# Performance work log

Hardware: AMD Instinct MI355X
Metric: run time of the kernel (lower is better)

Reference implementation:

```python
import jax, jax.numpy as jnp
import numpy as np

B, S, V, D = 64, 256, 50000, 300
NW, CL, CV, CD = 8192, 16, 500, 30
H, T, CH = 128, 17, 30


def setup_inputs() -> dict:
    key = jax.random.key(0)
    ks = jax.random.split(key, 32)
    f32 = jnp.float32
    def rn(k, shape, scale=0.1):
        return jax.random.normal(k, shape, dtype=f32) * scale
    inp = {}
    inp["char_emb"] = rn(ks[0], (CV, CD)).at[0].set(0.0)  # padding_idx=0
    inp["conv_w"] = rn(ks[1], (CH, CD, 3))  # OIH
    inp["conv_b"] = rn(ks[2], (CH,))
    inp["word_emb"] = rn(ks[3], (V, D))
    in0, in1 = D + CH, 2 * H
    inp["w_ih_l0"] = rn(ks[4], (2, 3 * H, in0))  # [dir, 3H, in]
    inp["w_hh_l0"] = rn(ks[5], (2, 3 * H, H))
    inp["b_ih_l0"] = rn(ks[6], (2, 3 * H))
    inp["b_hh_l0"] = rn(ks[7], (2, 3 * H))
    inp["w_ih_l1"] = rn(ks[8], (2, 3 * H, in1))
    inp["w_hh_l1"] = rn(ks[9], (2, 3 * H, H))
    inp["b_ih_l1"] = rn(ks[10], (2, 3 * H))
    inp["b_hh_l1"] = rn(ks[11], (2, 3 * H))
    inp["mlp_w1"] = rn(ks[12], (2 * H, H))
    inp["mlp_b1"] = rn(ks[13], (H,))
    inp["mlp_w2"] = rn(ks[14], (H, T))
    inp["mlp_b2"] = rn(ks[15], (T,))
    inp["crf_start"] = rn(ks[16], (T,))
    inp["crf_end"] = rn(ks[17], (T,))
    inp["crf_trans"] = rn(ks[18], (T, T))
    inp["batched_char_words"] = jax.random.randint(ks[19], (NW, CL), 0, CV)
    inp["batched_char_words_len"] = jax.random.randint(ks[20], (NW,), 1, CL + 1)
    inp["batched_char_word_index"] = jax.random.randint(ks[21], (B, S), 0, NW + 1)
    inp["batched_tokens"] = jax.random.randint(ks[22], (B, S), 0, V)
    inp["batched_tokens_len"] = jax.random.randint(ks[23], (B,), S // 2, S + 1)
    inp["target"] = jax.random.randint(ks[24], (B, S), 0, T)
    return inp


def _gru_dir(x, mask, w_ih, w_hh, b_ih, b_hh, reverse):
    # x: [B,S,I], mask: [B,S] bool. Masked (padded) steps carry hidden state
    # through unchanged, matching pack_padded_sequence semantics.
    xg = jnp.einsum('bsi,gi->sbg', x, w_ih) + b_ih  # [S,B,3H]
    m = mask.T  # [S,B]
    h0 = jnp.zeros((x.shape[0], w_hh.shape[1]), x.dtype)

    def step(h, inp):
        xt, mt = inp
        hg = h @ w_hh.T + b_hh
        xr, xz, xn = jnp.split(xt, 3, axis=-1)
        hr, hz, hn = jnp.split(hg, 3, axis=-1)
        r = jax.nn.sigmoid(xr + hr)
        z = jax.nn.sigmoid(xz + hz)
        n = jnp.tanh(xn + r * hn)
        hnew = (1.0 - z) * n + z * h
        h = jnp.where(mt[:, None], hnew, h)
        return h, h

    _, hs = jax.lax.scan(step, h0, (xg, m), reverse=reverse)
    return hs.transpose(1, 0, 2)  # [B,S,H]


def _bigru_layer(x, mask, w_ih, w_hh, b_ih, b_hh):
    fwd = _gru_dir(x, mask, w_ih[0], w_hh[0], b_ih[0], b_hh[0], False)
    bwd = _gru_dir(x, mask, w_ih[1], w_hh[1], b_ih[1], b_hh[1], True)
    return jnp.concatenate([fwd, bwd], axis=-1)


def _forward(char_emb, conv_w, conv_b, word_emb,
             w_ih_l0, w_hh_l0, b_ih_l0, b_hh_l0,
             w_ih_l1, w_hh_l1, b_ih_l1, b_hh_l1,
             mlp_w1, mlp_b1, mlp_w2, mlp_b2,
             crf_start, crf_end, crf_trans,
             batched_char_words, batched_char_word_index,
             batched_tokens, batched_tokens_len, target):
    # --- char CNN token encoder: conv1d(k=3, SAME) + relu + max-over-time ---
    ct = char_emb[batched_char_words]  # [NW,CL,CD]
    c = jax.lax.conv_general_dilated(ct.transpose(0, 2, 1), conv_w, (1,), 'SAME',
                                     dimension_numbers=('NCH', 'OIH', 'NCH'))
    c = jax.nn.relu(c + conv_b[None, :, None])
    tok_enc = jnp.max(c, axis=-1)  # [NW,CH]
    tok_enc = jnp.concatenate([jnp.zeros((1, tok_enc.shape[1]), tok_enc.dtype), tok_enc], axis=0)
    tok_idx = tok_enc[batched_char_word_index]  # [B,S,CH] (index 0 -> zeros)

    texts = jnp.concatenate([word_emb[batched_tokens], tok_idx], axis=-1)  # [B,S,D+CH]
    seq = batched_tokens.shape[1]
    mask = jnp.arange(seq)[None, :] < batched_tokens_len[:, None]  # [B,S]

    # --- 2-layer BiGRU ---
    h = _bigru_layer(texts, mask, w_ih_l0, w_hh_l0, b_ih_l0, b_hh_l0)
    h = _bigru_layer(h, mask, w_ih_l1, w_hh_l1, b_ih_l1, b_hh_l1)

    # --- MLP head -> emissions [B,S,17] ---
    h = jax.nn.relu(h @ mlp_w1 + mlp_b1)
    emissions = h @ mlp_w2 + mlp_b2

    # --- CRF negative log-likelihood, reduction='token_mean' ---
    maskf = mask.astype(emissions.dtype)
    emit_sc = jnp.take_along_axis(emissions, target[..., None], axis=-1)[..., 0]  # [B,S]
    trans_sc = crf_trans[target[:, :-1], target[:, 1:]]  # [B,S-1]
    score = crf_start[target[:, 0]] + emit_sc[:, 0]
    score = score + jnp.sum((trans_sc + emit_sc[:, 1:]) * maskf[:, 1:], axis=1)
    last_tags = jnp.take_along_axis(target, (batched_tokens_len - 1)[:, None], axis=1)[:, 0]
    score = score + crf_end[last_tags]

    alpha0 = crf_start[None, :] + emissions[:, 0]  # [B,T]
    em_rest = emissions[:, 1:].transpose(1, 0, 2)  # [S-1,B,T]
    m_rest = mask[:, 1:].T  # [S-1,B]

    def crf_step(alpha, inp):
        emit, mt = inp
        new = jax.nn.logsumexp(alpha[:, :, None] + crf_trans[None], axis=1) + emit
        return jnp.where(mt[:, None], new, alpha), None

    alpha, _ = jax.lax.scan(crf_step, alpha0, (em_rest, m_rest))
    log_z = jax.nn.logsumexp(alpha + crf_end[None, :], axis=1)
    llh = score - log_z
    return -(jnp.sum(llh) / jnp.sum(maskf))


def reference(char_emb, conv_w, conv_b, word_emb,
              w_ih_l0, w_hh_l0, b_ih_l0, b_hh_l0,
              w_ih_l1, w_hh_l1, b_ih_l1, b_hh_l1,
              mlp_w1, mlp_b1, mlp_w2, mlp_b2,
              crf_start, crf_end, crf_trans,
              batched_char_words, batched_char_words_len,
              batched_char_word_index, batched_tokens, batched_tokens_len, target):
    return _forward(char_emb, conv_w, conv_b, word_emb,
                    w_ih_l0, w_hh_l0, b_ih_l0, b_hh_l0,
                    w_ih_l1, w_hh_l1, b_ih_l1, b_hh_l1,
                    mlp_w1, mlp_b1, mlp_w2, mlp_b2,
                    crf_start, crf_end, crf_trans,
                    batched_char_words, batched_char_word_index,
                    batched_tokens, batched_tokens_len, target)
```

## Files before the change

### kernel.cpp

```cpp
#include <hip/hip_runtime.h>
#include <cstddef>

#define BATCH 64
#define SEQ   256
#define VOCAB 50000
#define DIM   300
#define NW    8192
#define CLEN  16
#define CDIM  30
#define CHC   30
#define HID   128
#define NT    17
#define IN0   (DIM + CHC)
#define IN0P  336
#define IN1   (2 * HID)
#define NPOS  (BATCH * SEQ)

constexpr size_t SZ_XG    = 2ull * BATCH * SEQ * 384;
constexpr size_t SZ_TEXTS = (size_t)NPOS * IN0P;
constexpr size_t SZ_H1    = (size_t)NPOS * 256;
constexpr size_t SZ_TOK   = 245792;
constexpr size_t SZ_EMIS  = (size_t)NPOS * NT;
constexpr size_t SZ_WPAD  = 768ull * IN0P;
constexpr size_t OFF_XG    = 0;
constexpr size_t OFF_TEXTS = OFF_XG + SZ_XG;
constexpr size_t OFF_H1    = OFF_TEXTS + SZ_TEXTS;
constexpr size_t OFF_TOK   = OFF_H1 + SZ_H1;
constexpr size_t OFF_EMIS  = OFF_TOK + SZ_TOK;
constexpr size_t OFF_WPAD  = OFF_EMIS + SZ_EMIS;
constexpr size_t OFF_LLH   = OFF_WPAD + SZ_WPAD;

__device__ __forceinline__ float sigm(float x) {
    return 1.f / (1.f + __expf(-x));
}
__device__ __forceinline__ float tanh_fast(float x) {
    x = fminf(fmaxf(x, -15.f), 15.f);
    float e = __expf(-2.f * x);
    return (1.f - e) / (1.f + e);
}
__device__ __forceinline__ float quad_sum(float x) {
    int y = __builtin_amdgcn_update_dpp(0, __float_as_int(x), 0xB1, 0xF, 0xF, false);
    x += __int_as_float(y);
    y = __builtin_amdgcn_update_dpp(0, __float_as_int(x), 0x4E, 0xF, 0xF, false);
    x += __int_as_float(y);
    return x;
}

__global__ __launch_bounds__(256) void char_conv_k(
    const float* __restrict__ char_emb,
    const float* __restrict__ conv_w,
    const float* __restrict__ conv_b,
    const int*   __restrict__ words,
    float* __restrict__ tok_enc)
{
    __shared__ __align__(16) float cs[8][CLEN][CDIM];
    __shared__ float wsm[CHC * CDIM * 3];
    __shared__ float bs[CHC];
    int n0 = blockIdx.x * 8;
    int tid = threadIdx.x;
    for (int e = tid; e < CHC * CDIM * 3; e += 256) wsm[e] = conv_w[e];
    if (tid < CHC) bs[tid] = conv_b[tid];
    for (int e = tid; e < 8 * CLEN * CDIM; e += 256) {
        int wi = e / (CLEN * CDIM);
        int rem = e - wi * (CLEN * CDIM);
        int l = rem / CDIM;
        int i = rem - l * CDIM;
        int ci = words[(n0 + wi) * CLEN + l];
        cs[wi][l][i] = char_emb[ci * CDIM + i];
    }
    __syncthreads();
    int wi = tid >> 5;
    int o = tid & 31;
    if (o < CHC) {
        float best = -1e30f;
        for (int l = 0; l < CLEN; l++) {
            float s = 0.f;
            #pragma unroll
            for (int k = 0; k < 3; k++) {
                int ll = l + k - 1;
                if (ll >= 0 && ll < CLEN) {
                    #pragma unroll
                    for (int i = 0; i < CDIM; i++)
                        s += cs[wi][ll][i] * wsm[(o * CDIM + i) * 3 + k];
                }
            }
            best = fmaxf(best, s);
        }
        tok_enc[(size_t)(n0 + wi + 1) * CDIM + o] = fmaxf(best + bs[o], 0.f);
    }
}

__global__ __launch_bounds__(128) void build_texts_k(
    const float* __restrict__ word_emb,
    const float* __restrict__ tok_enc,
    const int*   __restrict__ tokens,
    const int*   __restrict__ widx,
    float* __restrict__ texts)
{
    int p = blockIdx.x;
    int tok = tokens[p];
    int ci = widx[p];
    float* o = texts + (size_t)p * IN0P;
    const float* wr = word_emb + (size_t)tok * DIM;
    const float* tr = tok_enc + (size_t)ci * CDIM;
    for (int c = threadIdx.x; c < IN0P; c += 128)
        o[c] = (c < DIM) ? wr[c] : (c < IN0 ? tr[c - DIM] : 0.f);
}

__global__ __launch_bounds__(64) void pad_w_k(
    const float* __restrict__ w, float* __restrict__ wp)
{
    int r = blockIdx.x;
    for (int c = threadIdx.x; c < IN0P; c += 64)
        wp[(size_t)r * IN0P + c] = (c < IN0) ? w[(size_t)r * IN0 + c] : 0.f;
}

#define GBM 128
#define GBN 128
#define GBK 16
__global__ __launch_bounds__(256, 3) void gemm_xg_k(
    const float* __restrict__ A,
    const float* __restrict__ W,
    const float* __restrict__ bias,
    float* __restrict__ out,
    int K)
{
    __shared__ __align__(16) float As[2][GBK][GBM];
    __shared__ __align__(16) float Ws[2][GBK][GBN];
    int tid = threadIdx.x;
    int n0 = blockIdx.x * GBN;
    int m0 = blockIdx.y * GBM;
    int lrow = tid >> 1;
    int lk = (tid & 1) * 8;
    int ty = tid >> 4;
    int tx = tid & 15;

    const float* ap = A + (size_t)(m0 + lrow) * K + lk;
    const float* wpt = W + (size_t)(n0 + lrow) * K + lk;

    float acc[8][8];
    #pragma unroll
    for (int i = 0; i < 8; i++)
        #pragma unroll
        for (int j = 0; j < 8; j++) acc[i][j] = 0.f;

    float4 a0 = *(const float4*)(ap);
    float4 a1 = *(const float4*)(ap + 4);
    float4 w0 = *(const float4*)(wpt);
    float4 w1 = *(const float4*)(wpt + 4);
    {
        float* as = &As[0][lk][lrow];
        as[0*GBM] = a0.x; as[1*GBM] = a0.y; as[2*GBM] = a0.z; as[3*GBM] = a0.w;
        as[4*GBM] = a1.x; as[5*GBM] = a1.y; as[6*GBM] = a1.z; as[7*GBM] = a1.w;
        float* wsp = &Ws[0][lk][lrow];
        wsp[0*GBN] = w0.x; wsp[1*GBN] = w0.y; wsp[2*GBN] = w0.z; wsp[3*GBN] = w0.w;
        wsp[4*GBN] = w1.x; wsp[5*GBN] = w1.y; wsp[6*GBN] = w1.z; wsp[7*GBN] = w1.w;
    }
    __syncthreads();

    int nk = K / GBK;
    int cur = 0;
    for (int it = 1; it < nk; it++) {
        const float* apn = ap + it * GBK;
        const float* wpn = wpt + it * GBK;
        a0 = *(const float4*)(apn);
        a1 = *(const float4*)(apn + 4);
        w0 = *(const float4*)(wpn);
        w1 = *(const float4*)(wpn + 4);
        #pragma unroll
        for (int k = 0; k < GBK; k++) {
            float4 va0 = *(const float4*)&As[cur][k][ty * 8];
            float4 va1 = *(const float4*)&As[cur][k][ty * 8 + 4];
            float4 vb0 = *(const float4*)&Ws[cur][k][tx * 4];
            float4 vb1 = *(const float4*)&Ws[cur][k][64 + tx * 4];
            float av[8] = {va0.x, va0.y, va0.z, va0.w, va1.x, va1.y, va1.z, va1.w};
            float bv[8] = {vb0.x, vb0.y, vb0.z, vb0.w, vb1.x, vb1.y, vb1.z, vb1.w};
            #pragma unroll
            for (int i = 0; i < 8; i++)
                #pragma unroll
                for (int j = 0; j < 8; j++)
                    acc[i][j] += av[i] * bv[j];
        }
        int nb = cur ^ 1;
        {
            float* as = &As[nb][lk][lrow];
            as[0*GBM] = a0.x; as[1*GBM] = a0.y; as[2*GBM] = a0.z; as[3*GBM] = a0.w;
            as[4*GBM] = a1.x; as[5*GBM] = a1.y; as[6*GBM] = a1.z; as[7*GBM] = a1.w;
            float* wsp = &Ws[nb][lk][lrow];
            wsp[0*GBN] = w0.x; wsp[1*GBN] = w0.y; wsp[2*GBN] = w0.z; wsp[3*GBN] = w0.w;
            wsp[4*GBN] = w1.x; wsp[5*GBN] = w1.y; wsp[6*GBN] = w1.z; wsp[7*GBN] = w1.w;
        }
        __syncthreads();
        cur = nb;
    }
    #pragma unroll
    for (int k = 0; k < GBK; k++) {
        float4 va0 = *(const float4*)&As[cur][k][ty * 8];
        float4 va1 = *(const float4*)&As[cur][k][ty * 8 + 4];
        float4 vb0 = *(const float4*)&Ws[cur][k][tx * 4];
        float4 vb1 = *(const float4*)&Ws[cur][k][64 + tx * 4];
        float av[8] = {va0.x, va0.y, va0.z, va0.w, va1.x, va1.y, va1.z, va1.w};
        float bv[8] = {vb0.x, vb0.y, vb0.z, vb0.w, vb1.x, vb1.y, vb1.z, vb1.w};
        #pragma unroll
        for (int i = 0; i < 8; i++)
            #pragma unroll
            for (int j = 0; j < 8; j++)
                acc[i][j] += av[i] * bv[j];
    }

    int c0 = n0 + tx * 4;
    int d = (c0 >= 384) ? 1 : 0;
    int g0 = c0 - d * 384;
    float4 bb0 = *(const float4*)(bias + c0);
    float4 bb1 = *(const float4*)(bias + c0 + 64);
    int mbase = m0 + ty * 8;
    #pragma unroll
    for (int i = 0; i < 8; i++) {
        int m = mbase + i;
        int b = m >> 8;
        int t = m & 255;
        float* op = out + (((size_t)(d * BATCH + b) * SEQ + t) * 384);
        float4 r0, r1;
        r0.x = acc[i][0] + bb0.x; r0.y = acc[i][1] + bb0.y;
        r0.z = acc[i][2] + bb0.z; r0.w = acc[i][3] + bb0.w;
        r1.x = acc[i][4] + bb1.x; r1.y = acc[i][5] + bb1.y;
        r1.z = acc[i][6] + bb1.z; r1.w = acc[i][7] + bb1.w;
        *(float4*)(op + g0) = r0;
        *(float4*)(op + g0 + 64) = r1;
    }
}

__global__ __launch_bounds__(512, 2) void gru_rec_k(
    const float* __restrict__ xg,
    const float* __restrict__ w_hh,
    const float* __restrict__ b_hh,
    const int*   __restrict__ lens,
    float* __restrict__ out)
{
    int d = blockIdx.x & 1;
    int b = blockIdx.x >> 1;
    int i = threadIdx.x;
    int e = i >> 2;
    int c = i & 3;
    __shared__ __align__(16) float hS[2][HID];

    int rR = e, rZ = HID + e, rN = 2 * HID + e;
    const float* wbR = w_hh + ((size_t)d * 384 + rR) * HID + 32 * c;
    const float* wbZ = w_hh + ((size_t)d * 384 + rZ) * HID + 32 * c;
    const float* wbN = w_hh + ((size_t)d * 384 + rN) * HID + 32 * c;
    float4 wR[8], wZ[8], wN[8];
    #pragma unroll
    for (int q = 0; q < 8; q++) {
        int m = (q + c) & 7;
        wR[q] = *(const float4*)(wbR + 4 * m);
        wZ[q] = *(const float4*)(wbZ + 4 * m);
        wN[q] = *(const float4*)(wbN + 4 * m);
    }
    float bhR = b_hh[d * 384 + rR];
    float bhZ = b_hh[d * 384 + rZ];
    float bhN = b_hh[d * 384 + rN];
    int len = lens[b];

    if (i < HID) { hS[0][i] = 0.f; }
    float hold = 0.f;
    __syncthreads();

    const float* xgb = xg + ((size_t)(d * BATCH + b)) * SEQ * 384;
    float* outb = out + (size_t)b * SEQ * 256 + d * HID;

    int t0 = d ? (SEQ - 1) : 0;
    float xvR = xgb[(size_t)t0 * 384 + rR];
    float xvZ = xgb[(size_t)t0 * 384 + rZ];
    float xvN = xgb[(size_t)t0 * 384 + rN];
    int tPrev = 0;

    for (int s = 0; s < SEQ; s++) {
        int t = d ? (SEQ - 1 - s) : s;
        if (s && c == 0) outb[(size_t)tPrev * 256 + e] = hold;
        int sn = (s + 1 < SEQ) ? (s + 1) : s;
        int tn = d ? (SEQ - 1 - sn) : sn;
        float nxvR = xgb[(size_t)tn * 384 + rR];
        float nxvZ = xgb[(size_t)tn * 384 + rZ];
        float nxvN = xgb[(size_t)tn * 384 + rN];

        const float4* hb = (const float4*)hS[s & 1] + 8 * c;
        float sR = 0.f, sZ = 0.f, sN = 0.f;
        #pragma unroll
        for (int q = 0; q < 8; q++) {
            int m = (q + c) & 7;
            float4 hv = hb[m];
            sR += wR[q].x * hv.x + wR[q].y * hv.y + wR[q].z * hv.z + wR[q].w * hv.w;
            sZ += wZ[q].x * hv.x + wZ[q].y * hv.y + wZ[q].z * hv.z + wZ[q].w * hv.w;
            sN += wN[q].x * hv.x + wN[q].y * hv.y + wN[q].z * hv.z + wN[q].w * hv.w;
        }
        sR = quad_sum(sR);
        sZ = quad_sum(sZ);
        sN = quad_sum(sN);

        float r = sigm(xvR + sR + bhR);
        float z = sigm(xvZ + sZ + bhZ);
        float n = tanh_fast(xvN + r * (sN + bhN));
        float hnew = (1.f - z) * n + z * hold;
        hold = (t < len) ? hnew : hold;
        if (c == 0) hS[(s & 1) ^ 1][e] = hold;
        tPrev = t;
        xvR = nxvR; xvZ = nxvZ; xvN = nxvN;
        __syncthreads();
    }
    if (c == 0) outb[(size_t)tPrev * 256 + e] = hold;
}

__global__ __launch_bounds__(128) void mlp_emis_k(
    const float* __restrict__ h1,
    const float* __restrict__ w1,
    const float* __restrict__ b1,
    const float* __restrict__ w2,
    const float* __restrict__ b2,
    float* __restrict__ emis)
{
    __shared__ __align__(16) float hrow[8 * 256];
    __shared__ float hid[8][HID];
    int p0 = blockIdx.x * 8;
    int tid = threadIdx.x;
    for (int e = tid; e < 8 * 256; e += 128)
        hrow[e] = h1[(size_t)p0 * 256 + e];
    __syncthreads();
    float acc[8];
    float bb = b1[tid];
    #pragma unroll
    for (int i = 0; i < 8; i++) acc[i] = bb;
    for (int k = 0; k < 256; k++) {
        float wv = w1[k * HID + tid];
        #pragma unroll
        for (int i = 0; i < 8; i++) acc[i] += hrow[i * 256 + k] * wv;
    }
    #pragma unroll
    for (int i = 0; i < 8; i++) hid[i][tid] = fmaxf(acc[i], 0.f);
    __syncthreads();
    for (int idx = tid; idx < 8 * NT; idx += 128) {
        int pos = idx / NT;
        int tg = idx - pos * NT;
        float a = b2[tg];
        for (int k = 0; k < HID; k++) a += hid[pos][k] * w2[k * NT + tg];
        emis[(size_t)(p0 + pos) * NT + tg] = a;
    }
}

__global__ __launch_bounds__(64) void crf_k(
    const float* __restrict__ emis,
    const float* __restrict__ start,
    const float* __restrict__ endv,
    const float* __restrict__ trans,
    const int*   __restrict__ target,
    const int*   __restrict__ lens,
    float* __restrict__ llh)
{
    int b = blockIdx.x;
    int tid = threadIdx.x;
    __shared__ float tr[NT * NT];
    __shared__ float aSh[NT];
    __shared__ float scoreSh;
    for (int e = tid; e < NT * NT; e += 64) tr[e] = trans[e];
    __syncthreads();
    int len = lens[b];
    const int* tgt = target + b * SEQ;
    const float* eb = emis + (size_t)b * SEQ * NT;

    float part = 0.f;
    for (int t = 1 + tid; t < SEQ; t += 64) {
        if (t < len) {
            int tp = tgt[t - 1], tc = tgt[t];
            part += tr[tp * NT + tc] + eb[(size_t)t * NT + tc];
        }
    }
    #pragma unroll
    for (int off = 32; off > 0; off >>= 1)
        part += __shfl_down(part, off, 64);
    if (tid == 0) {
        int t0 = tgt[0];
        scoreSh = part + start[t0] + eb[t0] + endv[tgt[len - 1]];
    }

    float a = (tid < NT) ? (start[tid] + eb[tid]) : 0.f;
    for (int t = 1; t < SEQ; t++) {
        if (tid < NT) aSh[tid] = a;
        __syncthreads();
        if (t < len && tid < NT) {
            float m = -1e30f;
            #pragma unroll
            for (int i = 0; i < NT; i++)
                m = fmaxf(m, aSh[i] + tr[i * NT + tid]);
            float ssum = 0.f;
            #pragma unroll
            for (int i = 0; i < NT; i++)
                ssum += __expf(aSh[i] + tr[i * NT + tid] - m);
            a = m + __logf(ssum) + eb[(size_t)t * NT + tid];
        }
        __syncthreads();
    }
    float v = (tid < NT) ? (a + endv[tid]) : -1e30f;
    float m = v;
    #pragma unroll
    for (int off = 32; off > 0; off >>= 1)
        m = fmaxf(m, __shfl_down(m, off, 64));
    m = __shfl(m, 0, 64);
    float e = (tid < NT) ? __expf(v - m) : 0.f;
    #pragma unroll
    for (int off = 32; off > 0; off >>= 1)
        e += __shfl_down(e, off, 64);
    if (tid == 0) {
        float logz = m + __logf(e);
        llh[b] = scoreSh - logz;
    }
}

__global__ __launch_bounds__(64) void finalize_k(
    const float* __restrict__ llh,
    const int*   __restrict__ lens,
    float* __restrict__ out)
{
    int tid = threadIdx.x;
    float s = llh[tid];
    float lf = (float)lens[tid];
    #pragma unroll
    for (int off = 32; off > 0; off >>= 1) {
        s += __shfl_down(s, off, 64);
        lf += __shfl_down(lf, off, 64);
    }
    if (tid == 0) out[0] = -(s / lf);
}

extern "C" void kernel_launch(void* const* d_in, const int* in_sizes, int n_in,
                              void* d_out, int out_size, void* d_ws, size_t ws_size,
                              hipStream_t stream) {
    const float* char_emb = (const float*)d_in[0];
    const float* conv_w   = (const float*)d_in[1];
    const float* conv_b   = (const float*)d_in[2];
    const float* word_emb = (const float*)d_in[3];
    const float* w_ih_l0  = (const float*)d_in[4];
    const float* w_hh_l0  = (const float*)d_in[5];
    const float* b_ih_l0  = (const float*)d_in[6];
    const float* b_hh_l0  = (const float*)d_in[7];
    const float* w_ih_l1  = (const float*)d_in[8];
    const float* w_hh_l1  = (const float*)d_in[9];
    const float* b_ih_l1  = (const float*)d_in[10];
    const float* b_hh_l1  = (const float*)d_in[11];
    const float* mlp_w1   = (const float*)d_in[12];
    const float* mlp_b1   = (const float*)d_in[13];
    const float* mlp_w2   = (const float*)d_in[14];
    const float* mlp_b2   = (const float*)d_in[15];
    const float* crf_start= (const float*)d_in[16];
    const float* crf_end  = (const float*)d_in[17];
    const float* crf_trans= (const float*)d_in[18];
    const int* bcw   = (const int*)d_in[19];
    const int* bcwi  = (const int*)d_in[21];
    const int* btok  = (const int*)d_in[22];
    const int* blen  = (const int*)d_in[23];
    const int* target= (const int*)d_in[24];

    float* ws    = (float*)d_ws;
    float* xg    = ws + OFF_XG;
    float* texts = ws + OFF_TEXTS;
    float* h0    = texts;
    float* h1    = ws + OFF_H1;
    float* tok   = ws + OFF_TOK;
    float* emis  = ws + OFF_EMIS;
    float* wpad  = ws + OFF_WPAD;
    float* llh   = ws + OFF_LLH;

    hipMemsetAsync(tok, 0, CDIM * sizeof(float), stream);
    pad_w_k<<<768, 64, 0, stream>>>(w_ih_l0, wpad);
    char_conv_k<<<NW / 8, 256, 0, stream>>>(char_emb, conv_w, conv_b, bcw, tok);
    build_texts_k<<<NPOS, 128, 0, stream>>>(word_emb, tok, btok, bcwi, texts);
    gemm_xg_k<<<dim3(768 / GBN, NPOS / GBM), 256, 0, stream>>>(texts, wpad, b_ih_l0, xg, IN0P);
    gru_rec_k<<<2 * BATCH, 512, 0, stream>>>(xg, w_hh_l0, b_hh_l0, blen, h0);
    gemm_xg_k<<<dim3(768 / GBN, NPOS / GBM), 256, 0, stream>>>(h0, w_ih_l1, b_ih_l1, xg, IN1);
    gru_rec_k<<<2 * BATCH, 512, 0, stream>>>(xg, w_hh_l1, b_hh_l1, blen, h1);
    mlp_emis_k<<<NPOS / 8, 128, 0, stream>>>(h1, mlp_w1, mlp_b1, mlp_w2, mlp_b2, emis);
    crf_k<<<BATCH, 64, 0, stream>>>(emis, crf_start, crf_end, crf_trans, target, blen, llh);
    finalize_k<<<1, 64, 0, stream>>>(llh, blen, (float*)d_out);
}
```

Measured before the change: 930.8 us.

## Split GRU hidden-dot across 8 lanes per unit pair and swizzle GEMM block order

After: 946.4 us. Within noise of the previous version (+1.7%).

```diff
diff --git a/kernel.cpp b/kernel.cpp
--- a/kernel.cpp
+++ b/kernel.cpp
@@ -38,12 +38,19 @@
     float e = __expf(-2.f * x);
     return (1.f - e) / (1.f + e);
 }
+__device__ __forceinline__ float dot4(float4 a, float4 b) {
+    return a.x * b.x + a.y * b.y + a.z * b.z + a.w * b.w;
+}
 __device__ __forceinline__ float quad_sum(float x) {
     int y = __builtin_amdgcn_update_dpp(0, __float_as_int(x), 0xB1, 0xF, 0xF, false);
     x += __int_as_float(y);
     y = __builtin_amdgcn_update_dpp(0, __float_as_int(x), 0x4E, 0xF, 0xF, false);
     x += __int_as_float(y);
     return x;
+}
+__device__ __forceinline__ float xor4_add(float x) {
+    int y = __builtin_amdgcn_ds_swizzle(__float_as_int(x), 0x101F);
+    return x + __int_as_float(y);
 }
 
 __global__ __launch_bounds__(256) void char_conv_k(
@@ -128,8 +135,13 @@
     __shared__ __align__(16) float As[2][GBK][GBM];
     __shared__ __align__(16) float Ws[2][GBK][GBN];
     int tid = threadIdx.x;
-    int n0 = blockIdx.x * GBN;
-    int m0 = blockIdx.y * GBM;
+    int B = blockIdx.y * gridDim.x + blockIdx.x;
+    int X = B & 7;
+    int idx = B >> 3;
+    int mt = X * 16 + idx / 6;
+    int nt = idx - (idx / 6) * 6;
+    int n0 = nt * GBN;
+    int m0 = mt * GBM;
     int lrow = tid >> 1;
     int lk = (tid & 1) * 8;
     int ty = tid >> 4;
@@ -240,28 +252,34 @@
     int d = blockIdx.x & 1;
     int b = blockIdx.x >> 1;
     int i = threadIdx.x;
-    int e = i >> 2;
-    int c = i & 3;
+    int c = i & 7;
+    int e2 = i >> 3;
+    int sel = c & 1;
+    int eSel = e2 + 64 * sel;
     __shared__ __align__(16) float hS[2][HID];
 
-    int rR = e, rZ = HID + e, rN = 2 * HID + e;
-    const float* wbR = w_hh + ((size_t)d * 384 + rR) * HID + 32 * c;
-    const float* wbZ = w_hh + ((size_t)d * 384 + rZ) * HID + 32 * c;
-    const float* wbN = w_hh + ((size_t)d * 384 + rN) * HID + 32 * c;
-    float4 wR[8], wZ[8], wN[8];
-    #pragma unroll
-    for (int q = 0; q < 8; q++) {
-        int m = (q + c) & 7;
-        wR[q] = *(const float4*)(wbR + 4 * m);
-        wZ[q] = *(const float4*)(wbZ + 4 * m);
-        wN[q] = *(const float4*)(wbN + 4 * m);
-    }
-    float bhR = b_hh[d * 384 + rR];
-    float bhZ = b_hh[d * 384 + rZ];
-    float bhN = b_hh[d * 384 + rN];
+    int mj[4];
+    #pragma unroll
+    for (int j = 0; j < 4; j++) mj[j] = (j + (c >> 1)) & 3;
+
+    const float* wb = w_hh + (size_t)d * 384 * HID;
+    float4 wR0[4], wZ0[4], wN0[4], wR1[4], wZ1[4], wN1[4];
+    #pragma unroll
+    for (int j = 0; j < 4; j++) {
+        int off = 16 * c + 4 * mj[j];
+        wR0[j] = *(const float4*)(wb + (size_t)(e2)       * HID + off);
+        wZ0[j] = *(const float4*)(wb + (size_t)(128 + e2) * HID + off);
+        wN0[j] = *(const float4*)(wb + (size_t)(256 + e2) * HID + off);
+        wR1[j] = *(const float4*)(wb + (size_t)(64 + e2)  * HID + off);
+        wZ1[j] = *(const float4*)(wb + (size_t)(192 + e2) * HID + off);
+        wN1[j] = *(const float4*)(wb + (size_t)(320 + e2) * HID + off);
+    }
+    float bhR = b_hh[d * 384 + eSel];
+    float bhZ = b_hh[d * 384 + 128 + eSel];
+    float bhN = b_hh[d * 384 + 256 + eSel];
     int len = lens[b];
 
-    if (i < HID) { hS[0][i] = 0.f; }
+    if (i < HID) hS[0][i] = 0.f;
     float hold = 0.f;
     __syncthreads();
 
@@ -269,45 +287,55 @@
     float* outb = out + (size_t)b * SEQ * 256 + d * HID;
 
     int t0 = d ? (SEQ - 1) : 0;
-    float xvR = xgb[(size_t)t0 * 384 + rR];
-    float xvZ = xgb[(size_t)t0 * 384 + rZ];
-    float xvN = xgb[(size_t)t0 * 384 + rN];
-    int tPrev = 0;
+    float xvR = xgb[(size_t)t0 * 384 + eSel];
+    float xvZ = xgb[(size_t)t0 * 384 + 128 + eSel];
+    float xvN = xgb[(size_t)t0 * 384 + 256 + eSel];
+    int tPrev = t0;
+
+    int idxA = c * 4 + mj[0];
+    int idxB = c * 4 + mj[1];
+    int idxC = c * 4 + mj[2];
+    int idxD = c * 4 + mj[3];
 
     for (int s = 0; s < SEQ; s++) {
         int t = d ? (SEQ - 1 - s) : s;
-        if (s && c == 0) outb[(size_t)tPrev * 256 + e] = hold;
+        if (s && c < 2) outb[(size_t)tPrev * 256 + eSel] = hold;
         int sn = (s + 1 < SEQ) ? (s + 1) : s;
         int tn = d ? (SEQ - 1 - sn) : sn;
-        float nxvR = xgb[(size_t)tn * 384 + rR];
-        float nxvZ = xgb[(size_t)tn * 384 + rZ];
-        float nxvN = xgb[(size_t)tn * 384 + rN];
-
-        const float4* hb = (const float4*)hS[s & 1] + 8 * c;
-        float sR = 0.f, sZ = 0.f, sN = 0.f;
-        #pragma unroll
-        for (int q = 0; q < 8; q++) {
-            int m = (q + c) & 7;
-            float4 hv = hb[m];
-            sR += wR[q].x * hv.x + wR[q].y * hv.y + wR[q].z * hv.z + wR[q].w * hv.w;
-            sZ += wZ[q].x * hv.x + wZ[q].y * hv.y + wZ[q].z * hv.z + wZ[q].w * hv.w;
-            sN += wN[q].x * hv.x + wN[q].y * hv.y + wN[q].z * hv.z + wN[q].w * hv.w;
-        }
-        sR = quad_sum(sR);
-        sZ = quad_sum(sZ);
-        sN = quad_sum(sN);
+        float nxvR = xgb[(size_t)tn * 384 + eSel];
+        float nxvZ = xgb[(size_t)tn * 384 + 128 + eSel];
+        float nxvN = xgb[(size_t)tn * 384 + 256 + eSel];
+
+        const float4* hb = (const float4*)hS[s & 1];
+        float4 hv0 = hb[idxA];
+        float4 hv1 = hb[idxB];
+        float4 hv2 = hb[idxC];
+        float4 hv3 = hb[idxD];
+
+        float sR0 = dot4(wR0[0], hv0) + dot4(wR0[1], hv1) + dot4(wR0[2], hv2) + dot4(wR0[3], hv3);
+        float sZ0 = dot4(wZ0[0], hv0) + dot4(wZ0[1], hv1) + dot4(wZ0[2], hv2) + dot4(wZ0[3], hv3);
+        float sN0 = dot4(wN0[0], hv0) + dot4(wN0[1], hv1) + dot4(wN0[2], hv2) + dot4(wN0[3], hv3);
+        float sR1 = dot4(wR1[0], hv0) + dot4(wR1[1], hv1) + dot4(wR1[2], hv2) + dot4(wR1[3], hv3);
+        float sZ1 = dot4(wZ1[0], hv0) + dot4(wZ1[1], hv1) + dot4(wZ1[2], hv2) + dot4(wZ1[3], hv3);
+        float sN1 = dot4(wN1[0], hv0) + dot4(wN1[1], hv1) + dot4(wN1[2], hv2) + dot4(wN1[3], hv3);
+
+        sR0 = quad_sum(sR0); sZ0 = quad_sum(sZ0); sN0 = quad_sum(sN0);
+        sR1 = quad_sum(sR1); sZ1 = quad_sum(sZ1); sN1 = quad_sum(sN1);
+        float sR = xor4_add(sel ? sR1 : sR0);
+        float sZ = xor4_add(sel ? sZ1 : sZ0);
+        float sN = xor4_add(sel ? sN1 : sN0);
 
         float r = sigm(xvR + sR + bhR);
         float z = sigm(xvZ + sZ + bhZ);
         float n = tanh_fast(xvN + r * (sN + bhN));
         float hnew = (1.f - z) * n + z * hold;
         hold = (t < len) ? hnew : hold;
-        if (c == 0) hS[(s & 1) ^ 1][e] = hold;
+        if (c < 2) hS[(s & 1) ^ 1][eSel] = hold;
         tPrev = t;
         xvR = nxvR; xvZ = nxvZ; xvN = nxvN;
         __syncthreads();
     }
-    if (c == 0) outb[(size_t)tPrev * 256 + e] = hold;
+    if (c < 2) outb[(size_t)tPrev * 256 + eSel] = hold;
 }
 
 __global__ __launch_bounds__(128) void mlp_emis_k(
```
